# Kernel tuning notes

Hardware: AMD Instinct MI355X
Metric: run time of the kernel (lower is better)

## Reference

```python
import jax, jax.numpy as jnp
import numpy as np

LEAKY_SLOPE = 0.2
DENSITY = 0.05


def setup_inputs() -> dict:
    key = jax.random.key(0)
    k1, k2, k3, k4, k5, k6 = jax.random.split(key, 6)
    N, F_in, F_out = 8192, 128, 64
    h = jax.random.normal(k1, (N, F_in), dtype=jnp.float32)
    # Linear(in, out, bias=False) weight is [out, in]
    W = jax.random.normal(k2, (F_out, F_in), dtype=jnp.float32) * (1.0 / np.sqrt(F_in))
    a_left = jax.random.normal(k3, (F_out,), dtype=jnp.float32) * 0.1
    a_right = jax.random.normal(k4, (F_out,), dtype=jnp.float32) * 0.1
    vals = jax.random.uniform(k5, (N, N), dtype=jnp.float32)
    keep = jax.random.uniform(k6, (N, N)) < DENSITY
    adj = jnp.where(keep, vals, 0.0)  # raw adjacency; self-loops added in reference
    return {"h": h, "W": W, "a_left": a_left, "a_right": a_right, "adj": adj}


def reference(h, W, a_left, a_right, adj):
    N = adj.shape[0]
    A = adj + jnp.eye(N, dtype=adj.dtype)          # A = adjacency + I (self-loops)
    mask = jnp.abs(A) > 0                          # valued-mask support
    Wh = h @ W.T                                   # [N, F_out]
    e_left = Wh @ a_left                           # [N]
    e_right = Wh @ a_right                         # [N]
    e = e_left[:, None] + e_right[None, :]         # [N, N] additive scores
    e = jnp.where(e >= 0, e, LEAKY_SLOPE * e)      # LeakyReLU(0.2)
    e = jnp.where(mask, e, -jnp.inf)               # masked_fill(mask==0, -inf)
    attention = jax.nn.softmax(e, axis=1) * A      # valued masking post-softmax
    # dropout p=0.0 -> identity (eval-mode reference)
    return attention @ Wh                          # [N, F_out]
```

## Files before the change

kernel.cpp:

```cpp
#include <hip/hip_runtime.h>
#include <hip/hip_bf16.h>
#include <hip/hip_fp16.h>

#define N    8192
#define FIN  128
#define FOUT 64
#define LEAKY 0.2f
#define CAP  640
#define LOG2E 1.44269504088896340736f

struct alignas(8) Ent { unsigned joff; float w; };

__global__ __launch_bounds__(256) void wh_eLR_kernel(
    const float* __restrict__ h, const float* __restrict__ Wm,
    const float* __restrict__ aL, const float* __restrict__ aR,
    __half* __restrict__ Whh, float* __restrict__ eL2, float* __restrict__ eR2)
{
    __shared__ float sW[FOUT][FIN + 1];
    __shared__ float sh[4][FIN];
    const int t = threadIdx.x;
    const int rbase = blockIdx.x * 4;

    for (int idx = t; idx < FOUT * FIN; idx += 256)
        sW[idx >> 7][idx & 127] = Wm[idx];
    for (int idx = t; idx < 4 * FIN; idx += 256)
        sh[idx >> 7][idx & 127] = h[(size_t)(rbase + (idx >> 7)) * FIN + (idx & 127)];
    __syncthreads();

    const int wv = t >> 6, f = t & 63;
    const int row = rbase + wv;
    float acc = 0.f;
    #pragma unroll 16
    for (int k = 0; k < FIN; ++k) acc += sh[wv][k] * sW[f][k];
    Whh[(size_t)row * FOUT + f] = __float2half_rn(acc);

    float vl = acc * aL[f];
    float vr = acc * aR[f];
    #pragma unroll
    for (int d = 32; d > 0; d >>= 1) {
        vl += __shfl_down(vl, d, 64);
        vr += __shfl_down(vr, d, 64);
    }
    if (f == 0) { eL2[row] = vl * LOG2E; eR2[row] = vr * LOG2E; }
}

__global__ __launch_bounds__(256) void gat_row_kernel(
    const float* __restrict__ adj, const __half* __restrict__ Whh,
    const float* __restrict__ eL2p, const float* __restrict__ eR2p,
    float* __restrict__ out)
{
    __shared__ Ent ent[4][CAP];
    const int t = threadIdx.x;
    const int wv = t >> 6;
    const int lane = t & 63;
    const int row = blockIdx.x * 4 + wv;

    const float el = eL2p[row];

    const float4* __restrict__ arow4 = (const float4*)(adj + (size_t)row * N);
    Ent* __restrict__ myent = ent[wv];

    const unsigned l7 = ((unsigned)lane * 4) << 7;
    const unsigned l7u[4] = {l7, l7 + 128, l7 + 256, l7 + 384};

    int base = 0;
    const int rc = row >> 8;

    #pragma unroll 4
    for (int c = 0; c < 32; ++c) {
        const int idx4 = c * 64 + lane;
        const float4 a4 = arow4[idx4];
        const float av[4] = {a4.x, a4.y, a4.z, a4.w};
        const unsigned cbits = ((unsigned)c) << 15;
        const bool cdiag = (c == rc);
        #pragma unroll
        for (int u = 0; u < 4; ++u) {
            float a = av[u];
            if (cdiag) {
                if ((cbits | l7u[u]) == ((unsigned)row << 7)) a += 1.0f;
            }
            const bool nz = (a != 0.f);
            const unsigned long long m = __ballot(nz);
            const int before = __builtin_amdgcn_mbcnt_hi(
                (unsigned)(m >> 32),
                __builtin_amdgcn_mbcnt_lo((unsigned)m, 0));
            if (nz) {
                Ent e; e.joff = cbits | l7u[u]; e.w = a;
                myent[base + before] = e;
            }
            base += (int)__popcll(m);
        }
    }
    const int cnt = min(base, CAP - 16);
    if (lane < 16) { myent[cnt + lane].joff = 0; myent[cnt + lane].w = 0.f; }

    asm volatile("s_waitcnt lgkmcnt(0)" ::: "memory");

    const char* __restrict__ er2b = (const char*)eR2p;
    float lsum = 0.f;
    for (int k = lane; k < cnt; k += 64) {
        const Ent e = myent[k];
        const float er = *(const float*)(er2b + (e.joff >> 5));
        float y = el + er;
        y = fmaxf(y, LEAKY * y);
        const float p = exp2f(y);
        myent[k].w = p * e.w;
        lsum += p;
    }
    #pragma unroll
    for (int d = 32; d > 0; d >>= 1) lsum += __shfl_down(lsum, d, 64);
    const float rz = 1.0f / __shfl(lsum, 0, 64);

    asm volatile("s_waitcnt lgkmcnt(0)" ::: "memory");

    const int g = lane >> 4;
    const int fb = (lane & 15) * 8;
    const int cnt16 = (cnt + 15) & ~15;
    float ax = 0.f, ay = 0.f, az = 0.f, aw = 0.f;
    float bx = 0.f, by = 0.f, bz = 0.f, bw = 0.f;
    float cx = 0.f, cy = 0.f, cz = 0.f, cw = 0.f;
    float dx = 0.f, dy = 0.f, dz = 0.f, dw = 0.f;
    const char* __restrict__ whb = (const char*)Whh;
    for (int k = g; k < cnt16; k += 16) {
        const Ent e0 = myent[k];
        const Ent e1 = myent[k + 4];
        const Ent e2 = myent[k + 8];
        const Ent e3 = myent[k + 12];
        const uint2 u0 = *(const uint2*)(whb + (e0.joff + fb));
        const uint2 u1 = *(const uint2*)(whb + (e1.joff + fb));
        const uint2 u2 = *(const uint2*)(whb + (e2.joff + fb));
        const uint2 u3 = *(const uint2*)(whb + (e3.joff + fb));
        const float2 f00 = __half22float2(*(const __half2*)&u0.x);
        const float2 f01 = __half22float2(*(const __half2*)&u0.y);
        const float2 f10 = __half22float2(*(const __half2*)&u1.x);
        const float2 f11 = __half22float2(*(const __half2*)&u1.y);
        const float2 f20 = __half22float2(*(const __half2*)&u2.x);
        const float2 f21 = __half22float2(*(const __half2*)&u2.y);
        const float2 f30 = __half22float2(*(const __half2*)&u3.x);
        const float2 f31 = __half22float2(*(const __half2*)&u3.y);
        ax += e0.w * f00.x; ay += e0.w * f00.y; az += e0.w * f01.x; aw += e0.w * f01.y;
        bx += e1.w * f10.x; by += e1.w * f10.y; bz += e1.w * f11.x; bw += e1.w * f11.y;
        cx += e2.w * f20.x; cy += e2.w * f20.y; cz += e2.w * f21.x; cw += e2.w * f21.y;
        dx += e3.w * f30.x; dy += e3.w * f30.y; dz += e3.w * f31.x; dw += e3.w * f31.y;
    }
    ax += bx; ay += by; az += bz; aw += bw;
    cx += dx; cy += dy; cz += dz; cw += dw;
    ax += cx; ay += cy; az += cz; aw += cw;
    #pragma unroll
    for (int d = 32; d >= 16; d >>= 1) {
        ax += __shfl_down(ax, d, 64);
        ay += __shfl_down(ay, d, 64);
        az += __shfl_down(az, d, 64);
        aw += __shfl_down(aw, d, 64);
    }
    if (lane < 16) {
        float4 r;
        r.x = ax * rz; r.y = ay * rz; r.z = az * rz; r.w = aw * rz;
        *(float4*)(out + (size_t)row * FOUT + (lane & 15) * 4) = r;
    }
}

extern "C" void kernel_launch(void* const* d_in, const int* in_sizes, int n_in,
                              void* d_out, int out_size, void* d_ws, size_t ws_size,
                              hipStream_t stream) {
    const float* h   = (const float*)d_in[0];
    const float* Wm  = (const float*)d_in[1];
    const float* aL  = (const float*)d_in[2];
    const float* aR  = (const float*)d_in[3];
    const float* adj = (const float*)d_in[4];
    float* outp = (float*)d_out;

    __half* Whh = (__half*)d_ws;
    float* eL2  = (float*)((char*)d_ws + (size_t)N * FOUT * 2);
    float* eR2  = eL2 + N;

    wh_eLR_kernel<<<N / 4, 256, 0, stream>>>(h, Wm, aL, aR, Whh, eL2, eR2);
    gat_row_kernel<<<N / 4, 256, 0, stream>>>(adj, Whh, eL2, eR2, outp);
}
```

Baseline: 86.30 us.

## Fuse softmax and aggregation per chunk with prefetched adjacency rows

The GAT row kernel now processes the adjacency row in 16 chunks of two float4 columns each. The next chunk's loads are prefetched while the current chunk is compacted into LDS. The exp scores and the weighted fp16 Wh gather are then accumulated immediately for that chunk's new entries. This replaces the separate compaction, exp and aggregation passes with one streaming loop, so adjacency loads overlap with the gather compute. In exchange, each exp is recomputed by 16 lanes, and the CAP clamp and padding are dropped, so a row with more entries than CAP can overflow LDS.

```diff
diff --git a/kernel.cpp b/kernel.cpp
--- a/kernel.cpp
+++ b/kernel.cpp
@@ -56,106 +56,112 @@
     const int row = blockIdx.x * 4 + wv;
 
     const float el = eL2p[row];
-
     const float4* __restrict__ arow4 = (const float4*)(adj + (size_t)row * N);
+    const char* __restrict__ er2b = (const char*)eR2p;
+    const char* __restrict__ whb  = (const char*)Whh;
     Ent* __restrict__ myent = ent[wv];
 
     const unsigned l7 = ((unsigned)lane * 4) << 7;
     const unsigned l7u[4] = {l7, l7 + 128, l7 + 256, l7 + 384};
-
-    int base = 0;
+    const unsigned row7 = ((unsigned)row) << 7;
     const int rc = row >> 8;
 
-    #pragma unroll 4
-    for (int c = 0; c < 32; ++c) {
-        const int idx4 = c * 64 + lane;
-        const float4 a4 = arow4[idx4];
-        const float av[4] = {a4.x, a4.y, a4.z, a4.w};
-        const unsigned cbits = ((unsigned)c) << 15;
-        const bool cdiag = (c == rc);
+    const int g  = lane >> 4;
+    const int fb = (lane & 15) * 8;
+
+    int base = 0, cs = 0;
+    float psum = 0.f;
+    float a0x = 0.f, a0y = 0.f, a0z = 0.f, a0w = 0.f;
+    float a1x = 0.f, a1y = 0.f, a1z = 0.f, a1w = 0.f;
+
+    float4 b0 = arow4[lane];
+    float4 b1 = arow4[64 + lane];
+
+    for (int ch = 0; ch < 16; ++ch) {
+        float4 n0, n1;
+        if (ch < 15) {
+            n0 = arow4[(2 * ch + 2) * 64 + lane];
+            n1 = arow4[(2 * ch + 3) * 64 + lane];
+        }
+
         #pragma unroll
-        for (int u = 0; u < 4; ++u) {
-            float a = av[u];
-            if (cdiag) {
-                if ((cbits | l7u[u]) == ((unsigned)row << 7)) a += 1.0f;
+        for (int cc = 0; cc < 2; ++cc) {
+            const int c = 2 * ch + cc;
+            const float4 a4 = cc ? b1 : b0;
+            const float av[4] = {a4.x, a4.y, a4.z, a4.w};
+            const unsigned cbits = ((unsigned)c) << 15;
+            const bool cdiag = (c == rc);
+            #pragma unroll
+            for (int u = 0; u < 4; ++u) {
+                float a = av[u];
+                if (cdiag) {
+                    if ((cbits | l7u[u]) == row7) a += 1.0f;
+                }
+                const bool nz = (a != 0.f);
+                const unsigned long long m = __ballot(nz);
+                const int before = __builtin_amdgcn_mbcnt_hi(
+                    (unsigned)(m >> 32),
+                    __builtin_amdgcn_mbcnt_lo((unsigned)m, 0));
+                if (nz) {
+                    Ent e; e.joff = cbits | l7u[u]; e.w = a;
+                    myent[base + before] = e;
+                }
+                base += (int)__popcll(m);
             }
-            const bool nz = (a != 0.f);
-            const unsigned long long m = __ballot(nz);
-            const int before = __builtin_amdgcn_mbcnt_hi(
-                (unsigned)(m >> 32),
-                __builtin_amdgcn_mbcnt_lo((unsigned)m, 0));
-            if (nz) {
-                Ent e; e.joff = cbits | l7u[u]; e.w = a;
-                myent[base + before] = e;
+        }
+
+        asm volatile("s_waitcnt lgkmcnt(0)" ::: "memory");
+
+        const int ce = base;
+        for (int k = cs + g; k < ce; k += 8) {
+            const Ent e0 = myent[k];
+            const float er0 = *(const float*)(er2b + (e0.joff >> 5));
+            float y0 = el + er0;
+            y0 = fmaxf(y0, LEAKY * y0);
+            const float p0 = exp2f(y0);
+            const uint2 u0 = *(const uint2*)(whb + (e0.joff + fb));
+            const float2 f00 = __half22float2(*(const __half2*)&u0.x);
+            const float2 f01 = __half22float2(*(const __half2*)&u0.y);
+            const float w0 = p0 * e0.w;
+            a0x += w0 * f00.x; a0y += w0 * f00.y;
+            a0z += w0 * f01.x; a0w += w0 * f01.y;
+            psum += p0;
+            const int k2 = k + 4;
+            if (k2 < ce) {
+                const Ent e1 = myent[k2];
+                const float er1 = *(const float*)(er2b + (e1.joff >> 5));
+                float y1 = el + er1;
+                y1 = fmaxf(y1, LEAKY * y1);
+                const float p1 = exp2f(y1);
+                const uint2 u1 = *(const uint2*)(whb + (e1.joff + fb));
+                const float2 f10 = __half22float2(*(const __half2*)&u1.x);
+                const float2 f11 = __half22float2(*(const __half2*)&u1.y);
+                const float w1 = p1 * e1.w;
+                a1x += w1 * f10.x; a1y += w1 * f10.y;
+                a1z += w1 * f11.x; a1w += w1 * f11.y;
+                psum += p1;
             }
-            base += (int)__popcll(m);
         }
+        cs = ce;
+        if (ch < 15) { b0 = n0; b1 = n1; }
     }
-    const int cnt = min(base, CAP - 16);
-    if (lane < 16) { myent[cnt + lane].joff = 0; myent[cnt + lane].w = 0.f; }
 
-    asm volatile("s_waitcnt lgkmcnt(0)" ::: "memory");
+    float tot = psum;
+    tot += __shfl_xor(tot, 16, 64);
+    tot += __shfl_xor(tot, 32, 64);
+    const float rz = 1.0f / tot;
 
-    const char* __restrict__ er2b = (const char*)eR2p;
-    float lsum = 0.f;
-    for (int k = lane; k < cnt; k += 64) {
-        const Ent e = myent[k];
-        const float er = *(const float*)(er2b + (e.joff >> 5));
-        float y = el + er;
-        y = fmaxf(y, LEAKY * y);
-        const float p = exp2f(y);
-        myent[k].w = p * e.w;
-        lsum += p;
-    }
-    #pragma unroll
-    for (int d = 32; d > 0; d >>= 1) lsum += __shfl_down(lsum, d, 64);
-    const float rz = 1.0f / __shfl(lsum, 0, 64);
-
-    asm volatile("s_waitcnt lgkmcnt(0)" ::: "memory");
-
-    const int g = lane >> 4;
-    const int fb = (lane & 15) * 8;
-    const int cnt16 = (cnt + 15) & ~15;
-    float ax = 0.f, ay = 0.f, az = 0.f, aw = 0.f;
-    float bx = 0.f, by = 0.f, bz = 0.f, bw = 0.f;
-    float cx = 0.f, cy = 0.f, cz = 0.f, cw = 0.f;
-    float dx = 0.f, dy = 0.f, dz = 0.f, dw = 0.f;
-    const char* __restrict__ whb = (const char*)Whh;
-    for (int k = g; k < cnt16; k += 16) {
-        const Ent e0 = myent[k];
-        const Ent e1 = myent[k + 4];
-        const Ent e2 = myent[k + 8];
-        const Ent e3 = myent[k + 12];
-        const uint2 u0 = *(const uint2*)(whb + (e0.joff + fb));
-        const uint2 u1 = *(const uint2*)(whb + (e1.joff + fb));
-        const uint2 u2 = *(const uint2*)(whb + (e2.joff + fb));
-        const uint2 u3 = *(const uint2*)(whb + (e3.joff + fb));
-        const float2 f00 = __half22float2(*(const __half2*)&u0.x);
-        const float2 f01 = __half22float2(*(const __half2*)&u0.y);
-        const float2 f10 = __half22float2(*(const __half2*)&u1.x);
-        const float2 f11 = __half22float2(*(const __half2*)&u1.y);
-        const float2 f20 = __half22float2(*(const __half2*)&u2.x);
-        const float2 f21 = __half22float2(*(const __half2*)&u2.y);
-        const float2 f30 = __half22float2(*(const __half2*)&u3.x);
-        const float2 f31 = __half22float2(*(const __half2*)&u3.y);
-        ax += e0.w * f00.x; ay += e0.w * f00.y; az += e0.w * f01.x; aw += e0.w * f01.y;
-        bx += e1.w * f10.x; by += e1.w * f10.y; bz += e1.w * f11.x; bw += e1.w * f11.y;
-        cx += e2.w * f20.x; cy += e2.w * f20.y; cz += e2.w * f21.x; cw += e2.w * f21.y;
-        dx += e3.w * f30.x; dy += e3.w * f30.y; dz += e3.w * f31.x; dw += e3.w * f31.y;
-    }
-    ax += bx; ay += by; az += bz; aw += bw;
-    cx += dx; cy += dy; cz += dz; cw += dw;
-    ax += cx; ay += cy; az += cz; aw += cw;
+    a0x += a1x; a0y += a1y; a0z += a1z; a0w += a1w;
     #pragma unroll
     for (int d = 32; d >= 16; d >>= 1) {
-        ax += __shfl_down(ax, d, 64);
-        ay += __shfl_down(ay, d, 64);
-        az += __shfl_down(az, d, 64);
-        aw += __shfl_down(aw, d, 64);
+        a0x += __shfl_down(a0x, d, 64);
+        a0y += __shfl_down(a0y, d, 64);
+        a0z += __shfl_down(a0z, d, 64);
+        a0w += __shfl_down(a0w, d, 64);
     }
     if (lane < 16) {
         float4 r;
-        r.x = ax * rz; r.y = ay * rz; r.z = az * rz; r.w = aw * rz;
+        r.x = a0x * rz; r.y = a0y * rz; r.z = a0z * rz; r.w = a0w * rz;
         *(float4*)(out + (size_t)row * FOUT + (lane & 15) * 4) = r;
     }
 }
```

New measurement: 89.32 us. 1.04x slower.

## Split each adjacency row across four waves with block-level reduction

Applied to the files above, without the earlier changes.

The GAT row kernel now processes one row per 256-thread block instead of one row per wave. Each wave compacts and aggregates a quarter of the row's columns, then partial softmax sums and feature accumulators are combined through shared memory after a block barrier. The aim is more blocks in flight and a shorter per-wave serial loop over the 256 MB adjacency stream, which gives more memory-level parallelism. In exchange it adds a __syncthreads and a cross-wave reduction per row. The per-wave capacity of 256 entries truncates if a quarter-row holds more than 240 nonzeros.

```diff
diff --git a/kernel.cpp b/kernel.cpp
--- a/kernel.cpp
+++ b/kernel.cpp
@@ -6,7 +6,7 @@
 #define FIN  128
 #define FOUT 64
 #define LEAKY 0.2f
-#define CAP  640
+#define CAPQ 256
 #define LOG2E 1.44269504088896340736f
 
 struct alignas(8) Ent { unsigned joff; float w; };
@@ -49,35 +49,39 @@
     const float* __restrict__ eL2p, const float* __restrict__ eR2p,
     float* __restrict__ out)
 {
-    __shared__ Ent ent[4][CAP];
+    __shared__ Ent ent[4][CAPQ];
+    __shared__ float4 facc[4][16];
+    __shared__ float fpsum[4];
+
     const int t = threadIdx.x;
     const int wv = t >> 6;
     const int lane = t & 63;
-    const int row = blockIdx.x * 4 + wv;
+    const int row = blockIdx.x;
 
     const float el = eL2p[row];
-
     const float4* __restrict__ arow4 = (const float4*)(adj + (size_t)row * N);
+    const char* __restrict__ er2b = (const char*)eR2p;
+    const char* __restrict__ whb  = (const char*)Whh;
     Ent* __restrict__ myent = ent[wv];
 
-    const unsigned l7 = ((unsigned)lane * 4) << 7;
+    const unsigned l7 = ((unsigned)((wv << 11) + lane * 4)) << 7;
     const unsigned l7u[4] = {l7, l7 + 128, l7 + 256, l7 + 384};
+    const unsigned row7 = ((unsigned)row) << 7;
+    const int rcl = (row >> 8) - (wv << 3);
 
     int base = 0;
-    const int rc = row >> 8;
 
-    #pragma unroll 4
-    for (int c = 0; c < 32; ++c) {
-        const int idx4 = c * 64 + lane;
-        const float4 a4 = arow4[idx4];
+    #pragma unroll
+    for (int c = 0; c < 8; ++c) {
+        const float4 a4 = arow4[(wv << 9) + c * 64 + lane];
         const float av[4] = {a4.x, a4.y, a4.z, a4.w};
         const unsigned cbits = ((unsigned)c) << 15;
-        const bool cdiag = (c == rc);
+        const bool cdiag = (c == rcl);
         #pragma unroll
         for (int u = 0; u < 4; ++u) {
             float a = av[u];
             if (cdiag) {
-                if ((cbits | l7u[u]) == ((unsigned)row << 7)) a += 1.0f;
+                if ((cbits + l7u[u]) == row7) a += 1.0f;
             }
             const bool nz = (a != 0.f);
             const unsigned long long m = __ballot(nz);
@@ -85,18 +89,17 @@
                 (unsigned)(m >> 32),
                 __builtin_amdgcn_mbcnt_lo((unsigned)m, 0));
             if (nz) {
-                Ent e; e.joff = cbits | l7u[u]; e.w = a;
+                Ent e; e.joff = cbits + l7u[u]; e.w = a;
                 myent[base + before] = e;
             }
             base += (int)__popcll(m);
         }
     }
-    const int cnt = min(base, CAP - 16);
+    const int cnt = min(base, CAPQ - 16);
     if (lane < 16) { myent[cnt + lane].joff = 0; myent[cnt + lane].w = 0.f; }
 
     asm volatile("s_waitcnt lgkmcnt(0)" ::: "memory");
 
-    const char* __restrict__ er2b = (const char*)eR2p;
     float lsum = 0.f;
     for (int k = lane; k < cnt; k += 64) {
         const Ent e = myent[k];
@@ -109,7 +112,7 @@
     }
     #pragma unroll
     for (int d = 32; d > 0; d >>= 1) lsum += __shfl_down(lsum, d, 64);
-    const float rz = 1.0f / __shfl(lsum, 0, 64);
+    if (lane == 0) fpsum[wv] = lsum;
 
     asm volatile("s_waitcnt lgkmcnt(0)" ::: "memory");
 
@@ -120,7 +123,6 @@
     float bx = 0.f, by = 0.f, bz = 0.f, bw = 0.f;
     float cx = 0.f, cy = 0.f, cz = 0.f, cw = 0.f;
     float dx = 0.f, dy = 0.f, dz = 0.f, dw = 0.f;
-    const char* __restrict__ whb = (const char*)Whh;
     for (int k = g; k < cnt16; k += 16) {
         const Ent e0 = myent[k];
         const Ent e1 = myent[k + 4];
@@ -154,9 +156,24 @@
         aw += __shfl_down(aw, d, 64);
     }
     if (lane < 16) {
+        float4 p; p.x = ax; p.y = ay; p.z = az; p.w = aw;
+        facc[wv][lane] = p;
+    }
+    __syncthreads();
+
+    if (t < 16) {
+        const float Z = fpsum[0] + fpsum[1] + fpsum[2] + fpsum[3];
+        const float rz = 1.0f / Z;
+        const float4 p0 = facc[0][t];
+        const float4 p1 = facc[1][t];
+        const float4 p2 = facc[2][t];
+        const float4 p3 = facc[3][t];
         float4 r;
-        r.x = ax * rz; r.y = ay * rz; r.z = az * rz; r.w = aw * rz;
-        *(float4*)(out + (size_t)row * FOUT + (lane & 15) * 4) = r;
+        r.x = (p0.x + p1.x + p2.x + p3.x) * rz;
+        r.y = (p0.y + p1.y + p2.y + p3.y) * rz;
+        r.z = (p0.z + p1.z + p2.z + p3.z) * rz;
+        r.w = (p0.w + p1.w + p2.w + p3.w) * rz;
+        *(float4*)(out + (size_t)row * FOUT + t * 4) = r;
     }
 }
 
@@ -175,5 +192,5 @@
     float* eR2  = eL2 + N;
 
     wh_eLR_kernel<<<N / 4, 256, 0, stream>>>(h, Wm, aL, aR, Whh, eL2, eR2);
-    gat_row_kernel<<<N / 4, 256, 0, stream>>>(adj, Whh, eL2, eR2, outp);
+    gat_row_kernel<<<N, 256, 0, stream>>>(adj, Whh, eL2, eR2, outp);
 }
```

Result: faster. 81.79 us (-5.2%).
